# Performance work log

Hardware: AMD Instinct MI355X
Metric: run time of the kernel (lower is better)

## Reference

```python
import jax, jax.numpy as jnp
import numpy as np

# DeepSeek-V2 MLA dims (one tensor-parallel shard of 8)
H = 5120          # hidden size
S = 2048          # seq len
B = 1
NH = 16           # 128 heads / 8 devices
Q_LORA = 1536
KV_LORA = 512
NOPE = 128
ROPE = 64
QK = NOPE + ROPE  # 192 per-head q/k dim
VD = 128          # v head dim
DEVICE_NUM = 8
EPS = 1e-6


def rms_norm(x, w):
    v = jnp.mean(jnp.square(x.astype(jnp.float32)), axis=-1, keepdims=True)
    return (x * jax.lax.rsqrt(v + EPS)).astype(x.dtype) * w


def rope_cos_sin(position_ids, dim=ROPE, base=10000.0):
    inv_freq = 1.0 / (base ** (jnp.arange(0, dim, 2, dtype=jnp.float32) / dim))
    freqs = position_ids.astype(jnp.float32)[..., None] * inv_freq       # [B,S,dim/2]
    emb = jnp.concatenate([freqs, freqs], axis=-1)                        # [B,S,dim]
    return jnp.cos(emb), jnp.sin(emb)


def apply_rope(x, cos, sin):
    # DeepSeek interleaved reorder: view(b,h,s,d//2,2).transpose(-1,-2).reshape
    b, h, s, d = x.shape
    x = x.reshape(b, h, s, d // 2, 2).transpose(0, 1, 2, 4, 3).reshape(b, h, s, d)
    x1, x2 = x[..., : d // 2], x[..., d // 2:]
    rot = jnp.concatenate([-x2, x1], axis=-1)
    return x * cos[:, None] + rot * sin[:, None]


def setup_inputs() -> dict:
    key = jax.random.key(0)
    ks = jax.random.split(key, 8)
    sc = 0.02
    hidden_states = jax.random.normal(ks[0], (B, S, H), dtype=jnp.float32)
    position_ids = jnp.arange(S, dtype=jnp.int64 if jax.config.jax_enable_x64 else jnp.int32)[None, :].repeat(B, 0)
    attention_mask = jnp.triu(jnp.full((S, S), -1e9, dtype=jnp.float32), 1)[None, None]
    return {
        "hidden_states": hidden_states,
        "position_ids": position_ids,
        "attention_mask": attention_mask,
        "ln_w": jnp.ones((H,), jnp.float32),
        "q_a_w": jax.random.normal(ks[1], (Q_LORA, H), jnp.float32) * sc,
        "q_a_ln_w": jnp.ones((Q_LORA,), jnp.float32),
        "q_b_w": jax.random.normal(ks[2], (NH * QK, Q_LORA), jnp.float32) * sc,
        "kv_a_w": jax.random.normal(ks[3], (KV_LORA + ROPE, H), jnp.float32) * sc,
        "kv_a_ln_w": jnp.ones((KV_LORA,), jnp.float32),
        "kv_b_w": jax.random.normal(ks[4], (NH * (NOPE + VD), KV_LORA), jnp.float32) * sc,
        "o_w": jax.random.normal(ks[5], (H, NH * VD), jnp.float32) * sc,
    }


def reference(hidden_states, position_ids, attention_mask, ln_w, q_a_w, q_a_ln_w,
              q_b_w, kv_a_w, kv_a_ln_w, kv_b_w, o_w):
    b, s, _ = hidden_states.shape
    residual = hidden_states * (1.0 / DEVICE_NUM)
    x = rms_norm(hidden_states, ln_w)

    # Q path: low-rank down-proj + RMSNorm + up-proj
    q = rms_norm(x @ q_a_w.T, q_a_ln_w) @ q_b_w.T                # [b,s,NH*QK]
    q = q.reshape(b, s, NH, QK).transpose(0, 2, 1, 3)            # [b,NH,s,QK]
    q_nope, q_pe = q[..., :NOPE], q[..., NOPE:]

    # KV path: compressed latent + shared rope key
    ckv = x @ kv_a_w.T                                           # [b,s,KV_LORA+ROPE]
    c_kv, k_pe = ckv[..., :KV_LORA], ckv[..., KV_LORA:]
    k_pe = k_pe.reshape(b, s, 1, ROPE).transpose(0, 2, 1, 3)     # [b,1,s,ROPE]
    kv = rms_norm(c_kv, kv_a_ln_w) @ kv_b_w.T                    # [b,s,NH*(NOPE+VD)]
    kv = kv.reshape(b, s, NH, NOPE + VD).transpose(0, 2, 1, 3)
    k_nope, v = kv[..., :NOPE], kv[..., NOPE:]

    cos, sin = rope_cos_sin(position_ids)
    q_pe = apply_rope(q_pe, cos, sin)
    k_pe = apply_rope(k_pe, cos, sin)

    k = jnp.concatenate([k_nope, jnp.broadcast_to(k_pe, (b, NH, s, ROPE))], axis=-1)
    qf = jnp.concatenate([q_nope, q_pe], axis=-1)

    scores = jnp.einsum('bhqd,bhkd->bhqk', qf, k) * (1.0 / np.sqrt(QK))
    scores = scores + attention_mask
    probs = jax.nn.softmax(scores, axis=-1)
    attn = jnp.einsum('bhqk,bhkd->bhqd', probs, v)               # [b,NH,s,VD]

    out = attn.transpose(0, 2, 1, 3).reshape(b, s, NH * VD) @ o_w.T
    hidden = residual + out
    return hidden.astype(jnp.float32), k.astype(jnp.float32), v.astype(jnp.float32)
```

## Files before the change

### kernel.cpp

```cpp
#include <hip/hip_runtime.h>
#include <math.h>

typedef unsigned short u16;
typedef unsigned int u32;
typedef __attribute__((ext_vector_type(8))) short short8;
typedef __attribute__((ext_vector_type(4))) float f32x4;

#define NHEADS 16
static const int S      = 2048;
static const int Hd     = 5120;
static const int QLORA  = 1536;
static const int KVLORA = 512;
static const int NQK    = 192;
static const int NVD    = 128;
static const int QDIM   = 3072;
static const int KVDIM  = 4096;
static const int NFUSE  = 2176;

__device__ __forceinline__ u16 f2bf(float f) {
    union { float f; u32 u; } v; v.f = f;
    u32 r = v.u + 0x7FFFu + ((v.u >> 16) & 1u);
    return (u16)(r >> 16);
}

__global__ void convert_bf16_kernel(const float* __restrict__ src, u16* __restrict__ dst,
                                    int n_src, int n_total) {
    int i = (blockIdx.x * 256 + threadIdx.x) * 4;
    if (i >= n_total) return;
    union { u16 h[4]; uint2 u; } p;
    if (i < n_src) {
        float4 v = *(const float4*)(src + i);
        p.h[0] = f2bf(v.x); p.h[1] = f2bf(v.y); p.h[2] = f2bf(v.z); p.h[3] = f2bf(v.w);
    } else {
        p.h[0] = p.h[1] = p.h[2] = p.h[3] = 0;
    }
    *(uint2*)(dst + i) = p.u;
}

__global__ void rmsnorm_bf16_kernel(const float* in, const float* __restrict__ w,
                                    u16* out, int D, int in_stride, int out_stride) {
    int row = blockIdx.x;
    const float* x = in + (size_t)row * in_stride;
    u16* y = out + (size_t)row * out_stride;
    float ss = 0.f;
    for (int i = threadIdx.x; i < D; i += blockDim.x) { float v = x[i]; ss += v * v; }
    #pragma unroll
    for (int off = 32; off > 0; off >>= 1) ss += __shfl_xor(ss, off);
    __shared__ float wsum[8];
    int wid = threadIdx.x >> 6, lane = threadIdx.x & 63;
    if (lane == 0) wsum[wid] = ss;
    __syncthreads();
    float tot = 0.f;
    int nw = blockDim.x >> 6;
    for (int i = 0; i < nw; ++i) tot += wsum[i];
    float scale = rsqrtf(tot / (float)D + 1e-6f);
    for (int i = threadIdx.x; i < D; i += blockDim.x) y[i] = f2bf(x[i] * scale * w[i]);
}

__global__ __launch_bounds__(256) void gemm_bf16_kernel(
    const u16* __restrict__ A, const u16* __restrict__ B, float* __restrict__ C,
    int M, int N, int K, const float* __restrict__ resid) {
    __shared__ u16 As[4][128 * 32];
    __shared__ u16 Bs[4][128 * 32];

    const int lin = blockIdx.x + blockIdx.y * gridDim.x;
    const int nwg = gridDim.x * gridDim.y;
    const int xcd = lin & 7, off = lin >> 3;
    const int q = nwg >> 3, r = nwg & 7;
    const int wg = (xcd < r ? xcd * (q + 1) : r * (q + 1) + (xcd - r) * q) + off;
    const int bm = (wg % gridDim.y) * 128;
    const int bn = (wg / gridDim.y) * 128;

    const int tid = threadIdx.x;
    const int w = tid >> 6, lane = tid & 63;
    const int wr = w >> 1, wc = w & 1;
    const int fr = lane & 15, kg = lane >> 4;

    f32x4 acc[4][4];
    #pragma unroll
    for (int i = 0; i < 4; ++i)
        #pragma unroll
        for (int j = 0; j < 4; ++j) acc[i][j] = (f32x4){0.f, 0.f, 0.f, 0.f};

    const int srow = lane >> 2;
    const int scol = (lane & 3) * 8;
    const u16* Ap0 = A + (size_t)(bm + w * 32 + srow) * K + scol;
    const u16* Ap1 = Ap0 + (size_t)16 * K;
    const u16* Bp0 = B + (size_t)(bn + w * 32 + srow) * K + scol;
    const u16* Bp1 = Bp0 + (size_t)16 * K;
    const int ld0 = (w * 32) * 32;
    const int ld1 = (w * 32 + 16) * 32;

#define GSTAGE(buf, kk) do {                                                                  \
    __builtin_amdgcn_global_load_lds(                                                         \
        (const __attribute__((address_space(1))) void*)(Ap0 + (kk)),                          \
        (__attribute__((address_space(3))) void*)&As[buf][ld0], 16, 0, 0);                    \
    __builtin_amdgcn_global_load_lds(                                                         \
        (const __attribute__((address_space(1))) void*)(Ap1 + (kk)),                          \
        (__attribute__((address_space(3))) void*)&As[buf][ld1], 16, 0, 0);                    \
    __builtin_amdgcn_global_load_lds(                                                         \
        (const __attribute__((address_space(1))) void*)(Bp0 + (kk)),                          \
        (__attribute__((address_space(3))) void*)&Bs[buf][ld0], 16, 0, 0);                    \
    __builtin_amdgcn_global_load_lds(                                                         \
        (const __attribute__((address_space(1))) void*)(Bp1 + (kk)),                          \
        (__attribute__((address_space(3))) void*)&Bs[buf][ld1], 16, 0, 0);                    \
  } while (0)

#define GCOMP(buf) do {                                                                       \
    short8 af[4], bfr[4];                                                                     \
    _Pragma("unroll")                                                                         \
    for (int i = 0; i < 4; ++i) {                                                             \
      af[i]  = *(const short8*)&As[buf][(wr * 64 + i * 16 + fr) * 32 + kg * 8];               \
      bfr[i] = *(const short8*)&Bs[buf][(wc * 64 + i * 16 + fr) * 32 + kg * 8];               \
    }                                                                                         \
    _Pragma("unroll")                                                                         \
    for (int mi = 0; mi < 4; ++mi)                                                            \
      _Pragma("unroll")                                                                       \
      for (int ni = 0; ni < 4; ++ni)                                                          \
        acc[mi][ni] = __builtin_amdgcn_mfma_f32_16x16x32_bf16(af[mi], bfr[ni],                \
                                                              acc[mi][ni], 0, 0, 0);         \
  } while (0)

    const int nk = K >> 5;
    GSTAGE(0, 0);
    GSTAGE(1, 32);
    for (int kt = 0; kt < nk; ++kt) {
        if (kt + 2 < nk) {
            GSTAGE((kt + 2) & 3, (kt + 2) << 5);
            asm volatile("s_waitcnt vmcnt(8)" ::: "memory");
        } else if (kt + 1 < nk) {
            asm volatile("s_waitcnt vmcnt(4)" ::: "memory");
        } else {
            asm volatile("s_waitcnt vmcnt(0)" ::: "memory");
        }
        __builtin_amdgcn_s_barrier();
        GCOMP(kt & 3);
    }
#undef GSTAGE
#undef GCOMP

    #pragma unroll
    for (int mi = 0; mi < 4; ++mi)
        #pragma unroll
        for (int ni = 0; ni < 4; ++ni)
            #pragma unroll
            for (int r2 = 0; r2 < 4; ++r2) {
                int row = bm + wr * 64 + mi * 16 + kg * 4 + r2;
                int col = bn + wc * 64 + ni * 16 + fr;
                size_t idx = (size_t)row * N + col;
                float v = acc[mi][ni][r2];
                if (resid) v += resid[idx] * 0.125f;
                C[idx] = v;
            }
}

__global__ void prep_q_kernel(const float* __restrict__ Qb, const int* __restrict__ pos,
                              u16* __restrict__ Qbf) {
    const int s = blockIdx.x;
    const int t = threadIdx.x;
    const float* qrow = Qb + (size_t)s * QDIM;
    {
        int i = t * 4;
        int hh = i >> 7, d = i & 127;
        float4 v = *(const float4*)(qrow + hh * NQK + d);
        u16 p[4] = {f2bf(v.x), f2bf(v.y), f2bf(v.z), f2bf(v.w)};
        *(uint2*)(Qbf + ((size_t)hh * S + s) * NQK + d) = *(uint2*)p;
    }
    {
        int hh = t >> 5, j = t & 31;
        float ps = (float)pos[s];
        float inv_freq = 1.0f / powf(10000.0f, (float)j * (1.0f / 32.0f));
        float ang = ps * inv_freq;
        float c = cosf(ang), sn = sinf(ang);
        const float* pe = qrow + hh * NQK + 128;
        float a = pe[2 * j], b = pe[2 * j + 1];
        u16* dst = Qbf + ((size_t)hh * S + s) * NQK;
        dst[128 + j] = f2bf(a * c - b * sn);
        dst[160 + j] = f2bf(b * c + a * sn);
    }
}

__global__ void build_kv_kernel(const float* __restrict__ KV, const float* __restrict__ CKV,
                                int ckv_stride, const int* __restrict__ pos_ids,
                                float* __restrict__ Kout, float* __restrict__ Vout,
                                u16* __restrict__ Kbf) {
    int s = blockIdx.x;
    int t = threadIdx.x;
    __shared__ float kp[64];
    if (t < 32) {
        int j = t;
        float pos = (float)pos_ids[s];
        float inv_freq = 1.0f / powf(10000.0f, (float)j * (1.0f / 32.0f));
        float ang = pos * inv_freq;
        float c = cosf(ang), sn = sinf(ang);
        const float* kpe = CKV + (size_t)s * ckv_stride + KVLORA;
        float a = kpe[2 * j], b = kpe[2 * j + 1];
        kp[j] = a * c - b * sn;
        kp[32 + j] = b * c + a * sn;
    }
    __syncthreads();
    const float* kvrow = KV + (size_t)s * KVDIM;
    for (int i = t; i < NHEADS * NQK; i += 256) {
        int h = i / NQK, d = i % NQK;
        float v = (d < 128) ? kvrow[h * 256 + d] : kp[d - 128];
        size_t idx = ((size_t)h * S + s) * NQK + d;
        Kout[idx] = v;
        Kbf[idx] = f2bf(v);
    }
    for (int i = t; i < NHEADS * NVD; i += 256) {
        int h = i >> 7, d = i & 127;
        Vout[((size_t)h * S + s) * NVD + d] = kvrow[h * 256 + 128 + d];
    }
}

__global__ __launch_bounds__(256) void vt_kernel(const float* __restrict__ V, u16* __restrict__ Vt) {
    const int h = blockIdx.y;
    const int s0 = blockIdx.x * 64;
    const int t = threadIdx.x;
    __shared__ u16 T[64][132];
    #pragma unroll
    for (int j = 0; j < 8; ++j) {
        int f = t + j * 256;
        int row = f >> 5, c4 = f & 31;
        float4 v = *(const float4*)(V + ((size_t)h * S + s0 + row) * NVD + c4 * 4);
        u16 p[4] = {f2bf(v.x), f2bf(v.y), f2bf(v.z), f2bf(v.w)};
        *(uint2*)&T[row][c4 * 4] = *(uint2*)p;
    }
    __syncthreads();
    const int d = t >> 1, half = t & 1;
    #pragma unroll
    for (int c = 0; c < 4; ++c) {
        u16 tmp[8];
        #pragma unroll
        for (int e = 0; e < 8; ++e) tmp[e] = T[half * 32 + c * 8 + e][d];
        *(uint4*)(Vt + ((size_t)h * NVD + d) * S + s0 + half * 32 + c * 8) = *(uint4*)tmp;
    }
}

__global__ __launch_bounds__(256) void attn_mfma_kernel(
    const u16* __restrict__ Qbf, const u16* __restrict__ Kb,
    const u16* __restrict__ Vtb, u16* __restrict__ ATb) {
    const int h = blockIdx.y;
    const int q0 = blockIdx.x * 64;
    const int tid = threadIdx.x;
    const int w = tid >> 6, lane = tid & 63;
    const int fr = lane & 15, kg = lane >> 4;

    __shared__ __align__(16) u16 Ks[64 * 192];
    __shared__ __align__(16) u16 Vts[128 * 64];

    int kSrc[6], vSrc[4];
    #pragma unroll
    for (int i = 0; i < 6; ++i) {
        int D = (w * 6 + i) * 1024 + lane * 16;
        int row = D / 384, wb = D - row * 384;
        kSrc[i] = row * 384 + (wb ^ ((row & 7) << 4));
    }
    #pragma unroll
    for (int i = 0; i < 4; ++i) {
        int D = (w * 4 + i) * 1024 + lane * 16;
        int row = D >> 7, wb = D & 127;
        vSrc[i] = row * (S * 2) + (wb ^ ((row & 7) << 4));
    }
    const char* Kg = (const char*)(Kb + (size_t)h * S * NQK);
    const char* Vg = (const char*)(Vtb + (size_t)h * NVD * S);

    short8 qf[6];
    {
        const u16* qrow = Qbf + ((size_t)h * S + q0 + w * 16 + fr) * NQK;
        #pragma unroll
        for (int kb = 0; kb < 6; ++kb)
            qf[kb] = *(const short8*)(qrow + kb * 32 + kg * 8);
    }

    f32x4 o[8];
    #pragma unroll
    for (int ni = 0; ni < 8; ++ni) o[ni] = (f32x4){0.f, 0.f, 0.f, 0.f};
    float mrow = -1e30f, lrow = 0.f;
    const float scale = 0.0721687836487032f;
    const int qg = q0 + w * 16 + fr;
    const int swz = (fr & 7) << 4;

    for (int k0 = 0; k0 <= q0; k0 += 64) {
        __syncthreads();
        #pragma unroll
        for (int i = 0; i < 6; ++i)
            __builtin_amdgcn_global_load_lds(
                (const __attribute__((address_space(1))) void*)(Kg + (size_t)k0 * 384 + kSrc[i]),
                (__attribute__((address_space(3))) void*)((char*)Ks + (w * 6 + i) * 1024), 16, 0, 0);
        #pragma unroll
        for (int i = 0; i < 4; ++i)
            __builtin_amdgcn_global_load_lds(
                (const __attribute__((address_space(1))) void*)(Vg + (size_t)k0 * 2 + vSrc[i]),
                (__attribute__((address_space(3))) void*)((char*)Vts + (w * 4 + i) * 1024), 16, 0, 0);
        __syncthreads();

        f32x4 sacc[4];
        #pragma unroll
        for (int mi = 0; mi < 4; ++mi) sacc[mi] = (f32x4){0.f, 0.f, 0.f, 0.f};
        #pragma unroll
        for (int mi = 0; mi < 4; ++mi)
            #pragma unroll
            for (int kb = 0; kb < 6; ++kb) {
                const short8 kf = *(const short8*)((const char*)Ks +
                    (mi * 16 + fr) * 384 + ((kb * 64 + kg * 16) ^ swz));
                sacc[mi] = __builtin_amdgcn_mfma_f32_16x16x32_bf16(kf, qf[kb], sacc[mi], 0, 0, 0);
            }

        const bool diag = (k0 == q0);
        float p[4][4];
        float mx = -1e30f;
        #pragma unroll
        for (int mi = 0; mi < 4; ++mi)
            #pragma unroll
            for (int r = 0; r < 4; ++r) {
                float v = sacc[mi][r] * scale;
                if (diag && (k0 + mi * 16 + kg * 4 + r > qg)) v = -1e30f;
                p[mi][r] = v;
                mx = fmaxf(mx, v);
            }
        mx = fmaxf(mx, __shfl_xor(mx, 16));
        mx = fmaxf(mx, __shfl_xor(mx, 32));
        float mnew = fmaxf(mrow, mx);
        float corr = __expf(mrow - mnew);
        float psum = 0.f;
        #pragma unroll
        for (int mi = 0; mi < 4; ++mi)
            #pragma unroll
            for (int r = 0; r < 4; ++r) {
                float e = __expf(p[mi][r] - mnew);
                p[mi][r] = e;
                psum += e;
            }
        psum += __shfl_xor(psum, 16);
        psum += __shfl_xor(psum, 32);
        lrow = lrow * corr + psum;
        mrow = mnew;
        float corr_r[4];
        #pragma unroll
        for (int r = 0; r < 4; ++r) corr_r[r] = __shfl(corr, kg * 4 + r);
        #pragma unroll
        for (int ni = 0; ni < 8; ++ni) {
            o[ni][0] *= corr_r[0]; o[ni][1] *= corr_r[1];
            o[ni][2] *= corr_r[2]; o[ni][3] *= corr_r[3];
        }

        u32 pk0[4], pk1[4];
        #pragma unroll
        for (int mi = 0; mi < 4; ++mi) {
            pk0[mi] = (u32)f2bf(p[mi][0]) | ((u32)f2bf(p[mi][1]) << 16);
            pk1[mi] = (u32)f2bf(p[mi][2]) | ((u32)f2bf(p[mi][3]) << 16);
        }
        const int srcA = 2 * (kg & 1) * 16 + fr;
        const int srcB = srcA + 16;
        const int hsel = kg >> 1;
        short8 pa[2];
        #pragma unroll
        for (int ks = 0; ks < 2; ++ks) {
            u32 a0 = (u32)__shfl((int)pk0[ks * 2], srcA), b0 = (u32)__shfl((int)pk0[ks * 2 + 1], srcA);
            u32 a1 = (u32)__shfl((int)pk1[ks * 2], srcA), b1 = (u32)__shfl((int)pk1[ks * 2 + 1], srcA);
            u32 a2 = (u32)__shfl((int)pk0[ks * 2], srcB), b2 = (u32)__shfl((int)pk0[ks * 2 + 1], srcB);
            u32 a3 = (u32)__shfl((int)pk1[ks * 2], srcB), b3 = (u32)__shfl((int)pk1[ks * 2 + 1], srcB);
            union { u32 u[4]; short8 s8; } cvt;
            cvt.u[0] = hsel ? b0 : a0;
            cvt.u[1] = hsel ? b1 : a1;
            cvt.u[2] = hsel ? b2 : a2;
            cvt.u[3] = hsel ? b3 : a3;
            pa[ks] = cvt.s8;
        }

        #pragma unroll
        for (int ks = 0; ks < 2; ++ks)
            #pragma unroll
            for (int ni = 0; ni < 8; ++ni) {
                const short8 vf = *(const short8*)((const char*)Vts +
                    (ni * 16 + fr) * 128 + ((ks * 64 + kg * 16) ^ swz));
                o[ni] = __builtin_amdgcn_mfma_f32_16x16x32_bf16(pa[ks], vf, o[ni], 0, 0, 0);
            }
    }

    float inv = 1.f / lrow;
    float inv_r[4];
    #pragma unroll
    for (int r = 0; r < 4; ++r) inv_r[r] = __shfl(inv, kg * 4 + r);
    u16* outp = ATb + (size_t)(q0 + w * 16 + kg * 4) * (NHEADS * NVD) + h * NVD + fr;
    #pragma unroll
    for (int ni = 0; ni < 8; ++ni)
        #pragma unroll
        for (int r = 0; r < 4; ++r)
            outp[(size_t)r * (NHEADS * NVD) + ni * 16] = f2bf(o[ni][r] * inv_r[r]);
}

extern "C" void kernel_launch(void* const* d_in, const int* in_sizes, int n_in,
                              void* d_out, int out_size, void* d_ws, size_t ws_size,
                              hipStream_t stream) {
    (void)in_sizes; (void)n_in; (void)out_size; (void)ws_size;
    const float* hidden    = (const float*)d_in[0];
    const int*   pos       = (const int*)d_in[1];
    const float* ln_w      = (const float*)d_in[3];
    const float* q_a_w     = (const float*)d_in[4];
    const float* q_a_ln_w  = (const float*)d_in[5];
    const float* q_b_w     = (const float*)d_in[6];
    const float* kv_a_w    = (const float*)d_in[7];
    const float* kv_a_ln_w = (const float*)d_in[8];
    const float* kv_b_w    = (const float*)d_in[9];
    const float* o_w       = (const float*)d_in[10];

    float* OUT_H = (float*)d_out;
    float* OUT_K = OUT_H + (size_t)S * Hd;
    float* OUT_V = OUT_K + (size_t)NHEADS * S * NQK;

    char* ws = (char*)d_ws;
    u16*   o_wb    = (u16*)(ws);
    u16*   Wf      = (u16*)(ws + 20971520);
    u16*   Xb      = (u16*)(ws + 43253760);
    float* CF      = (float*)(ws + 64225280);
    u16*   QAn     = (u16*)(ws + 82055680);
    u16*   q_b_wb  = (u16*)(ws + 88347136);
    float* Qb      = (float*)(ws + 20971520);
    u16*   kv_b_wb = (u16*)(ws + 46137344);
    u16*   CKVN    = (u16*)(ws + 82055680);
    float* KV      = (float*)(ws + 84152832);
    u16*   Qbf     = (u16*)(ws + 50331648);
    u16*   Kbf     = (u16*)(ws + 20971520);
    u16*   Vtb     = (u16*)(ws + 33554432);
    u16*   ATb     = (u16*)(ws + 64225280);

    convert_bf16_kernel<<<(Hd * 2048 / 4 + 255) / 256, 256, 0, stream>>>(o_w, o_wb, Hd * 2048, Hd * 2048);
    convert_bf16_kernel<<<(QLORA * Hd / 4 + 255) / 256, 256, 0, stream>>>(q_a_w, Wf, QLORA * Hd, QLORA * Hd);
    convert_bf16_kernel<<<(640 * Hd / 4 + 255) / 256, 256, 0, stream>>>(kv_a_w, Wf + (size_t)QLORA * Hd, 576 * Hd, 640 * Hd);

    rmsnorm_bf16_kernel<<<S, 256, 0, stream>>>(hidden, ln_w, Xb, Hd, Hd, Hd);
    gemm_bf16_kernel<<<dim3(NFUSE / 128, S / 128), 256, 0, stream>>>(Xb, Wf, CF, S, NFUSE, Hd, nullptr);
    convert_bf16_kernel<<<(KVDIM * KVLORA / 4 + 255) / 256, 256, 0, stream>>>(kv_b_w, kv_b_wb, KVDIM * KVLORA, KVDIM * KVLORA);
    rmsnorm_bf16_kernel<<<S, 256, 0, stream>>>(CF, q_a_ln_w, QAn, QLORA, NFUSE, QLORA);
    convert_bf16_kernel<<<(QDIM * QLORA / 4 + 255) / 256, 256, 0, stream>>>(q_b_w, q_b_wb, QDIM * QLORA, QDIM * QLORA);
    gemm_bf16_kernel<<<dim3(QDIM / 128, S / 128), 256, 0, stream>>>(QAn, q_b_wb, Qb, S, QDIM, QLORA, nullptr);
    rmsnorm_bf16_kernel<<<S, 256, 0, stream>>>(CF + QLORA, kv_a_ln_w, CKVN, KVLORA, NFUSE, KVLORA);
    gemm_bf16_kernel<<<dim3(KVDIM / 128, S / 128), 256, 0, stream>>>(CKVN, kv_b_wb, KV, S, KVDIM, KVLORA, nullptr);
    prep_q_kernel<<<S, 512, 0, stream>>>(Qb, pos, Qbf);
    build_kv_kernel<<<S, 256, 0, stream>>>(KV, CF + QLORA, NFUSE, pos, OUT_K, OUT_V, Kbf);
    vt_kernel<<<dim3(S / 64, NHEADS), 256, 0, stream>>>(OUT_V, Vtb);
    attn_mfma_kernel<<<dim3(S / 64, NHEADS), 256, 0, stream>>>(Qbf, Kbf, Vtb, ATb);
    gemm_bf16_kernel<<<dim3(Hd / 128, S / 128), 256, 0, stream>>>(ATb, o_wb, OUT_H, S, Hd, NHEADS * NVD, hidden);
}
```

Before: 445.2 us.

## Emit bf16 intermediates from GEMMs, fuse K/V build with V transpose, add BM=64 tiles

```diff
diff --git a/kernel.cpp b/kernel.cpp
--- a/kernel.cpp
+++ b/kernel.cpp
@@ -22,6 +22,9 @@
     u32 r = v.u + 0x7FFFu + ((v.u >> 16) & 1u);
     return (u16)(r >> 16);
 }
+__device__ __forceinline__ float bf2f(u16 h) {
+    union { u32 u; float f; } v; v.u = (u32)h << 16; return v.f;
+}
 
 __global__ void convert_bf16_kernel(const float* __restrict__ src, u16* __restrict__ dst,
                                     int n_src, int n_total) {
@@ -57,114 +60,148 @@
     for (int i = threadIdx.x; i < D; i += blockDim.x) y[i] = f2bf(x[i] * scale * w[i]);
 }
 
-__global__ __launch_bounds__(256) void gemm_bf16_kernel(
-    const u16* __restrict__ A, const u16* __restrict__ B, float* __restrict__ C,
+__global__ void rmsnorm_bf16in_kernel(const u16* in, const float* __restrict__ w,
+                                      u16* out, int D, int in_stride, int out_stride) {
+    int row = blockIdx.x;
+    const u16* x = in + (size_t)row * in_stride;
+    u16* y = out + (size_t)row * out_stride;
+    float ss = 0.f;
+    for (int i = threadIdx.x; i < D; i += blockDim.x) { float v = bf2f(x[i]); ss += v * v; }
+    #pragma unroll
+    for (int off = 32; off > 0; off >>= 1) ss += __shfl_xor(ss, off);
+    __shared__ float wsum[8];
+    int wid = threadIdx.x >> 6, lane = threadIdx.x & 63;
+    if (lane == 0) wsum[wid] = ss;
+    __syncthreads();
+    float tot = 0.f;
+    int nw = blockDim.x >> 6;
+    for (int i = 0; i < nw; ++i) tot += wsum[i];
+    float scale = rsqrtf(tot / (float)D + 1e-6f);
+    for (int i = threadIdx.x; i < D; i += blockDim.x) y[i] = f2bf(bf2f(x[i]) * scale * w[i]);
+}
+
+template<int BM, bool SWZ, bool OBF>
+__global__ __launch_bounds__(256) void gemm_k(
+    const u16* __restrict__ A, const u16* __restrict__ B, void* __restrict__ Cv,
     int M, int N, int K, const float* __restrict__ resid) {
-    __shared__ u16 As[4][128 * 32];
+    constexpr int MR = BM / 32;
+    __shared__ u16 As[4][BM * 32];
     __shared__ u16 Bs[4][128 * 32];
 
-    const int lin = blockIdx.x + blockIdx.y * gridDim.x;
-    const int nwg = gridDim.x * gridDim.y;
-    const int xcd = lin & 7, off = lin >> 3;
-    const int q = nwg >> 3, r = nwg & 7;
-    const int wg = (xcd < r ? xcd * (q + 1) : r * (q + 1) + (xcd - r) * q) + off;
-    const int bm = (wg % gridDim.y) * 128;
-    const int bn = (wg / gridDim.y) * 128;
+    int bm, bn;
+    if constexpr (SWZ) {
+        const int lin = blockIdx.x + blockIdx.y * gridDim.x;
+        const int nwg = gridDim.x * gridDim.y;
+        const int xcd = lin & 7, off = lin >> 3;
+        const int q = nwg >> 3, r = nwg & 7;
+        const int wg = (xcd < r ? xcd * (q + 1) : r * (q + 1) + (xcd - r) * q) + off;
+        bm = (wg % gridDim.y) * BM;
+        bn = (wg / gridDim.y) * 128;
+    } else {
+        bm = blockIdx.y * BM;
+        bn = blockIdx.x * 128;
+    }
 
     const int tid = threadIdx.x;
     const int w = tid >> 6, lane = tid & 63;
     const int wr = w >> 1, wc = w & 1;
     const int fr = lane & 15, kg = lane >> 4;
 
-    f32x4 acc[4][4];
-    #pragma unroll
-    for (int i = 0; i < 4; ++i)
+    f32x4 acc[MR][4];
+    #pragma unroll
+    for (int i = 0; i < MR; ++i)
         #pragma unroll
         for (int j = 0; j < 4; ++j) acc[i][j] = (f32x4){0.f, 0.f, 0.f, 0.f};
 
     const int srow = lane >> 2;
     const int scol = (lane & 3) * 8;
-    const u16* Ap0 = A + (size_t)(bm + w * 32 + srow) * K + scol;
+    const u16* Ap0 = A + (size_t)(bm + w * (BM / 4) + srow) * K + scol;
     const u16* Ap1 = Ap0 + (size_t)16 * K;
     const u16* Bp0 = B + (size_t)(bn + w * 32 + srow) * K + scol;
     const u16* Bp1 = Bp0 + (size_t)16 * K;
-    const int ld0 = (w * 32) * 32;
-    const int ld1 = (w * 32 + 16) * 32;
-
-#define GSTAGE(buf, kk) do {                                                                  \
-    __builtin_amdgcn_global_load_lds(                                                         \
-        (const __attribute__((address_space(1))) void*)(Ap0 + (kk)),                          \
-        (__attribute__((address_space(3))) void*)&As[buf][ld0], 16, 0, 0);                    \
-    __builtin_amdgcn_global_load_lds(                                                         \
-        (const __attribute__((address_space(1))) void*)(Ap1 + (kk)),                          \
-        (__attribute__((address_space(3))) void*)&As[buf][ld1], 16, 0, 0);                    \
-    __builtin_amdgcn_global_load_lds(                                                         \
-        (const __attribute__((address_space(1))) void*)(Bp0 + (kk)),                          \
-        (__attribute__((address_space(3))) void*)&Bs[buf][ld0], 16, 0, 0);                    \
-    __builtin_amdgcn_global_load_lds(                                                         \
-        (const __attribute__((address_space(1))) void*)(Bp1 + (kk)),                          \
-        (__attribute__((address_space(3))) void*)&Bs[buf][ld1], 16, 0, 0);                    \
-  } while (0)
-
-#define GCOMP(buf) do {                                                                       \
-    short8 af[4], bfr[4];                                                                     \
-    _Pragma("unroll")                                                                         \
-    for (int i = 0; i < 4; ++i) {                                                             \
-      af[i]  = *(const short8*)&As[buf][(wr * 64 + i * 16 + fr) * 32 + kg * 8];               \
-      bfr[i] = *(const short8*)&Bs[buf][(wc * 64 + i * 16 + fr) * 32 + kg * 8];               \
-    }                                                                                         \
-    _Pragma("unroll")                                                                         \
-    for (int mi = 0; mi < 4; ++mi)                                                            \
-      _Pragma("unroll")                                                                       \
-      for (int ni = 0; ni < 4; ++ni)                                                          \
-        acc[mi][ni] = __builtin_amdgcn_mfma_f32_16x16x32_bf16(af[mi], bfr[ni],                \
-                                                              acc[mi][ni], 0, 0, 0);         \
-  } while (0)
+    const int lda0 = (w * (BM / 4)) * 32;
+    const int lda1 = (w * (BM / 4) + 16) * 32;
+    const int ldb0 = (w * 32) * 32;
+    const int ldb1 = (w * 32 + 16) * 32;
+
+    auto STAGE = [&](int buf, int kk) {
+        __builtin_amdgcn_global_load_lds(
+            (const __attribute__((address_space(1))) void*)(Ap0 + kk),
+            (__attribute__((address_space(3))) void*)&As[buf][lda0], 16, 0, 0);
+        if constexpr (BM == 128)
+            __builtin_amdgcn_global_load_lds(
+                (const __attribute__((address_space(1))) void*)(Ap1 + kk),
+                (__attribute__((address_space(3))) void*)&As[buf][lda1], 16, 0, 0);
+        __builtin_amdgcn_global_load_lds(
+            (const __attribute__((address_space(1))) void*)(Bp0 + kk),
+            (__attribute__((address_space(3))) void*)&Bs[buf][ldb0], 16, 0, 0);
+        __builtin_amdgcn_global_load_lds(
+            (const __attribute__((address_space(1))) void*)(Bp1 + kk),
+            (__attribute__((address_space(3))) void*)&Bs[buf][ldb1], 16, 0, 0);
+    };
+    auto COMP = [&](int buf) {
+        short8 af[MR], bfr[4];
+        #pragma unroll
+        for (int i = 0; i < MR; ++i)
+            af[i] = *(const short8*)&As[buf][(wr * (BM / 2) + i * 16 + fr) * 32 + kg * 8];
+        #pragma unroll
+        for (int i = 0; i < 4; ++i)
+            bfr[i] = *(const short8*)&Bs[buf][(wc * 64 + i * 16 + fr) * 32 + kg * 8];
+        #pragma unroll
+        for (int mi = 0; mi < MR; ++mi)
+            #pragma unroll
+            for (int ni = 0; ni < 4; ++ni)
+                acc[mi][ni] = __builtin_amdgcn_mfma_f32_16x16x32_bf16(af[mi], bfr[ni],
+                                                                      acc[mi][ni], 0, 0, 0);
+    };
 
     const int nk = K >> 5;
-    GSTAGE(0, 0);
-    GSTAGE(1, 32);
+    STAGE(0, 0);
+    STAGE(1, 32);
     for (int kt = 0; kt < nk; ++kt) {
         if (kt + 2 < nk) {
-            GSTAGE((kt + 2) & 3, (kt + 2) << 5);
-            asm volatile("s_waitcnt vmcnt(8)" ::: "memory");
+            STAGE((kt + 2) & 3, (kt + 2) << 5);
+            if constexpr (BM == 128) asm volatile("s_waitcnt vmcnt(8)" ::: "memory");
+            else                     asm volatile("s_waitcnt vmcnt(6)" ::: "memory");
         } else if (kt + 1 < nk) {
-            asm volatile("s_waitcnt vmcnt(4)" ::: "memory");
+            if constexpr (BM == 128) asm volatile("s_waitcnt vmcnt(4)" ::: "memory");
+            else                     asm volatile("s_waitcnt vmcnt(3)" ::: "memory");
         } else {
             asm volatile("s_waitcnt vmcnt(0)" ::: "memory");
         }
         __builtin_amdgcn_s_barrier();
-        GCOMP(kt & 3);
-    }
-#undef GSTAGE
-#undef GCOMP
-
-    #pragma unroll
-    for (int mi = 0; mi < 4; ++mi)
+        COMP(kt & 3);
+    }
+
+    #pragma unroll
+    for (int mi = 0; mi < MR; ++mi)
         #pragma unroll
         for (int ni = 0; ni < 4; ++ni)
             #pragma unroll
             for (int r2 = 0; r2 < 4; ++r2) {
-                int row = bm + wr * 64 + mi * 16 + kg * 4 + r2;
+                int row = bm + wr * (BM / 2) + mi * 16 + kg * 4 + r2;
                 int col = bn + wc * 64 + ni * 16 + fr;
                 size_t idx = (size_t)row * N + col;
                 float v = acc[mi][ni][r2];
-                if (resid) v += resid[idx] * 0.125f;
-                C[idx] = v;
+                if constexpr (OBF) {
+                    ((u16*)Cv)[idx] = f2bf(v);
+                } else {
+                    if (resid) v += resid[idx] * 0.125f;
+                    ((float*)Cv)[idx] = v;
+                }
             }
 }
 
-__global__ void prep_q_kernel(const float* __restrict__ Qb, const int* __restrict__ pos,
+__global__ void prep_q_kernel(const u16* __restrict__ Qb, const int* __restrict__ pos,
                               u16* __restrict__ Qbf) {
     const int s = blockIdx.x;
     const int t = threadIdx.x;
-    const float* qrow = Qb + (size_t)s * QDIM;
+    const u16* qrow = Qb + (size_t)s * QDIM;
     {
         int i = t * 4;
         int hh = i >> 7, d = i & 127;
-        float4 v = *(const float4*)(qrow + hh * NQK + d);
-        u16 p[4] = {f2bf(v.x), f2bf(v.y), f2bf(v.z), f2bf(v.w)};
-        *(uint2*)(Qbf + ((size_t)hh * S + s) * NQK + d) = *(uint2*)p;
+        uint2 v = *(const uint2*)(qrow + hh * NQK + d);
+        *(uint2*)(Qbf + ((size_t)hh * S + s) * NQK + d) = v;
     }
     {
         int hh = t >> 5, j = t & 31;
@@ -172,59 +209,71 @@
         float inv_freq = 1.0f / powf(10000.0f, (float)j * (1.0f / 32.0f));
         float ang = ps * inv_freq;
         float c = cosf(ang), sn = sinf(ang);
-        const float* pe = qrow + hh * NQK + 128;
-        float a = pe[2 * j], b = pe[2 * j + 1];
+        const u16* pe = qrow + hh * NQK + 128;
+        float a = bf2f(pe[2 * j]), b = bf2f(pe[2 * j + 1]);
         u16* dst = Qbf + ((size_t)hh * S + s) * NQK;
         dst[128 + j] = f2bf(a * c - b * sn);
         dst[160 + j] = f2bf(b * c + a * sn);
     }
 }
 
-__global__ void build_kv_kernel(const float* __restrict__ KV, const float* __restrict__ CKV,
-                                int ckv_stride, const int* __restrict__ pos_ids,
-                                float* __restrict__ Kout, float* __restrict__ Vout,
-                                u16* __restrict__ Kbf) {
-    int s = blockIdx.x;
-    int t = threadIdx.x;
-    __shared__ float kp[64];
-    if (t < 32) {
-        int j = t;
-        float pos = (float)pos_ids[s];
+__global__ __launch_bounds__(256) void build_kv64_kernel(
+    const u16* __restrict__ KVb, const u16* __restrict__ CF,
+    const int* __restrict__ pos_ids,
+    float* __restrict__ Kout, float* __restrict__ Vout,
+    u16* __restrict__ Kbf, u16* __restrict__ Vtb) {
+    const int s0 = blockIdx.x * 64;
+    const int h  = blockIdx.y;
+    const int t  = threadIdx.x;
+    __shared__ u16 T[64][132];
+
+    #pragma unroll
+    for (int it = 0; it < 4; ++it) {
+        int i = t + it * 256;
+        int row = i >> 4, c8 = (i & 15) * 8;
+        int s = s0 + row;
+        union { uint4 u; u16 hx[8]; } v;
+        v.u = *(const uint4*)(KVb + (size_t)s * KVDIM + h * 256 + c8);
+        size_t kidx = ((size_t)h * S + s) * NQK + c8;
+        *(uint4*)(Kbf + kidx) = v.u;
+        float4 f0 = {bf2f(v.hx[0]), bf2f(v.hx[1]), bf2f(v.hx[2]), bf2f(v.hx[3])};
+        float4 f1 = {bf2f(v.hx[4]), bf2f(v.hx[5]), bf2f(v.hx[6]), bf2f(v.hx[7])};
+        *(float4*)(Kout + kidx) = f0;
+        *(float4*)(Kout + kidx + 4) = f1;
+    }
+    #pragma unroll
+    for (int it = 0; it < 4; ++it) {
+        int i = t + it * 256;
+        int row = i >> 4, c8 = (i & 15) * 8;
+        int s = s0 + row;
+        union { uint4 u; uint2 d[2]; u16 hx[8]; } v;
+        v.u = *(const uint4*)(KVb + (size_t)s * KVDIM + h * 256 + 128 + c8);
+        *(uint2*)&T[row][c8]     = v.d[0];
+        *(uint2*)&T[row][c8 + 4] = v.d[1];
+        size_t vidx = ((size_t)h * S + s) * NVD + c8;
+        float4 f0 = {bf2f(v.hx[0]), bf2f(v.hx[1]), bf2f(v.hx[2]), bf2f(v.hx[3])};
+        float4 f1 = {bf2f(v.hx[4]), bf2f(v.hx[5]), bf2f(v.hx[6]), bf2f(v.hx[7])};
+        *(float4*)(Vout + vidx) = f0;
+        *(float4*)(Vout + vidx + 4) = f1;
+    }
+    #pragma unroll
+    for (int it = 0; it < 8; ++it) {
+        int i = t + it * 256;
+        int row = i >> 5, j = i & 31;
+        int s = s0 + row;
+        float ps = (float)pos_ids[s];
         float inv_freq = 1.0f / powf(10000.0f, (float)j * (1.0f / 32.0f));
-        float ang = pos * inv_freq;
+        float ang = ps * inv_freq;
         float c = cosf(ang), sn = sinf(ang);
-        const float* kpe = CKV + (size_t)s * ckv_stride + KVLORA;
-        float a = kpe[2 * j], b = kpe[2 * j + 1];
-        kp[j] = a * c - b * sn;
-        kp[32 + j] = b * c + a * sn;
-    }
-    __syncthreads();
-    const float* kvrow = KV + (size_t)s * KVDIM;
-    for (int i = t; i < NHEADS * NQK; i += 256) {
-        int h = i / NQK, d = i % NQK;
-        float v = (d < 128) ? kvrow[h * 256 + d] : kp[d - 128];
-        size_t idx = ((size_t)h * S + s) * NQK + d;
-        Kout[idx] = v;
-        Kbf[idx] = f2bf(v);
-    }
-    for (int i = t; i < NHEADS * NVD; i += 256) {
-        int h = i >> 7, d = i & 127;
-        Vout[((size_t)h * S + s) * NVD + d] = kvrow[h * 256 + 128 + d];
-    }
-}
-
-__global__ __launch_bounds__(256) void vt_kernel(const float* __restrict__ V, u16* __restrict__ Vt) {
-    const int h = blockIdx.y;
-    const int s0 = blockIdx.x * 64;
-    const int t = threadIdx.x;
-    __shared__ u16 T[64][132];
-    #pragma unroll
-    for (int j = 0; j < 8; ++j) {
-        int f = t + j * 256;
-        int row = f >> 5, c4 = f & 31;
-        float4 v = *(const float4*)(V + ((size_t)h * S + s0 + row) * NVD + c4 * 4);
-        u16 p[4] = {f2bf(v.x), f2bf(v.y), f2bf(v.z), f2bf(v.w)};
-        *(uint2*)&T[row][c4 * 4] = *(uint2*)p;
+        u32 pr = *(const u32*)(CF + (size_t)s * NFUSE + QLORA + KVLORA + 2 * j);
+        float a = bf2f((u16)pr), b = bf2f((u16)(pr >> 16));
+        float k0 = a * c - b * sn;
+        float k1 = b * c + a * sn;
+        size_t kidx = ((size_t)h * S + s) * NQK;
+        Kout[kidx + 128 + j] = k0;
+        Kout[kidx + 160 + j] = k1;
+        Kbf[kidx + 128 + j] = f2bf(k0);
+        Kbf[kidx + 160 + j] = f2bf(k1);
     }
     __syncthreads();
     const int d = t >> 1, half = t & 1;
@@ -233,7 +282,7 @@
         u16 tmp[8];
         #pragma unroll
         for (int e = 0; e < 8; ++e) tmp[e] = T[half * 32 + c * 8 + e][d];
-        *(uint4*)(Vt + ((size_t)h * NVD + d) * S + s0 + half * 32 + c * 8) = *(uint4*)tmp;
+        *(uint4*)(Vtb + ((size_t)h * NVD + d) * S + s0 + half * 32 + c * 8) = *(uint4*)tmp;
     }
 }
 
@@ -413,34 +462,33 @@
     char* ws = (char*)d_ws;
     u16*   o_wb    = (u16*)(ws);
     u16*   Wf      = (u16*)(ws + 20971520);
+    u16*   Qbf     = (u16*)(ws + 20971520);
+    u16*   Vtb     = (u16*)(ws + 33554432);
     u16*   Xb      = (u16*)(ws + 43253760);
-    float* CF      = (float*)(ws + 64225280);
-    u16*   QAn     = (u16*)(ws + 82055680);
-    u16*   q_b_wb  = (u16*)(ws + 88347136);
-    float* Qb      = (float*)(ws + 20971520);
-    u16*   kv_b_wb = (u16*)(ws + 46137344);
-    u16*   CKVN    = (u16*)(ws + 82055680);
-    float* KV      = (float*)(ws + 84152832);
-    u16*   Qbf     = (u16*)(ws + 50331648);
-    u16*   Kbf     = (u16*)(ws + 20971520);
-    u16*   Vtb     = (u16*)(ws + 33554432);
-    u16*   ATb     = (u16*)(ws + 64225280);
+    u16*   Kbf     = (u16*)(ws + 43253760);
+    u16*   ATb     = (u16*)(ws + 55836672);
+    u16*   CF      = (u16*)(ws + 64225280);
+    u16*   QAn     = (u16*)(ws + 73138176);
+    u16*   CKVN    = (u16*)(ws + 73138176);
+    u16*   q_b_wb  = (u16*)(ws + 79429632);
+    u16*   kv_b_wb = (u16*)(ws + 79429632);
+    u16*   KVb     = (u16*)(ws + 88866816);
+    u16*   Qb      = (u16*)(ws + 105644032);
 
     convert_bf16_kernel<<<(Hd * 2048 / 4 + 255) / 256, 256, 0, stream>>>(o_w, o_wb, Hd * 2048, Hd * 2048);
     convert_bf16_kernel<<<(QLORA * Hd / 4 + 255) / 256, 256, 0, stream>>>(q_a_w, Wf, QLORA * Hd, QLORA * Hd);
     convert_bf16_kernel<<<(640 * Hd / 4 + 255) / 256, 256, 0, stream>>>(kv_a_w, Wf + (size_t)QLORA * Hd, 576 * Hd, 640 * Hd);
 
     rmsnorm_bf16_kernel<<<S, 256, 0, stream>>>(hidden, ln_w, Xb, Hd, Hd, Hd);
-    gemm_bf16_kernel<<<dim3(NFUSE / 128, S / 128), 256, 0, stream>>>(Xb, Wf, CF, S, NFUSE, Hd, nullptr);
+    gemm_k<128, true, true><<<dim3(NFUSE / 128, S / 128), 256, 0, stream>>>(Xb, Wf, CF, S, NFUSE, Hd, nullptr);
+    convert_bf16_kernel<<<(QDIM * QLORA / 4 + 255) / 256, 256, 0, stream>>>(q_b_w, q_b_wb, QDIM * QLORA, QDIM * QLORA);
+    rmsnorm_bf16in_kernel<<<S, 256, 0, stream>>>(CF, q_a_ln_w, QAn, QLORA, NFUSE, QLORA);
+    gemm_k<128, true, true><<<dim3(QDIM / 128, S / 128), 256, 0, stream>>>(QAn, q_b_wb, Qb, S, QDIM, QLORA, nullptr);
     convert_bf16_kernel<<<(KVDIM * KVLORA / 4 + 255) / 256, 256, 0, stream>>>(kv_b_w, kv_b_wb, KVDIM * KVLORA, KVDIM * KVLORA);
-    rmsnorm_bf16_kernel<<<S, 256, 0, stream>>>(CF, q_a_ln_w, QAn, QLORA, NFUSE, QLORA);
-    convert_bf16_kernel<<<(QDIM * QLORA / 4 + 255) / 256, 256, 0, stream>>>(q_b_w, q_b_wb, QDIM * QLORA, QDIM * QLORA);
-    gemm_bf16_kernel<<<dim3(QDIM / 128, S / 128), 256, 0, stream>>>(QAn, q_b_wb, Qb, S, QDIM, QLORA, nullptr);
-    rmsnorm_bf16_kernel<<<S, 256, 0, stream>>>(CF + QLORA, kv_a_ln_w, CKVN, KVLORA, NFUSE, KVLORA);
-    gemm_bf16_kernel<<<dim3(KVDIM / 128, S / 128), 256, 0, stream>>>(CKVN, kv_b_wb, KV, S, KVDIM, KVLORA, nullptr);
+    rmsnorm_bf16in_kernel<<<S, 256, 0, stream>>>(CF + QLORA, kv_a_ln_w, CKVN, KVLORA, NFUSE, KVLORA);
+    gemm_k<64, false, true><<<dim3(KVDIM / 128, S / 64), 256, 0, stream>>>(CKVN, kv_b_wb, KVb, S, KVDIM, KVLORA, nullptr);
     prep_q_kernel<<<S, 512, 0, stream>>>(Qb, pos, Qbf);
-    build_kv_kernel<<<S, 256, 0, stream>>>(KV, CF + QLORA, NFUSE, pos, OUT_K, OUT_V, Kbf);
-    vt_kernel<<<dim3(S / 64, NHEADS), 256, 0, stream>>>(OUT_V, Vtb);
+    build_kv64_kernel<<<dim3(S / 64, NHEADS), 256, 0, stream>>>(KVb, CF, pos, OUT_K, OUT_V, Kbf, Vtb);
     attn_mfma_kernel<<<dim3(S / 64, NHEADS), 256, 0, stream>>>(Qbf, Kbf, Vtb, ATb);
-    gemm_bf16_kernel<<<dim3(Hd / 128, S / 128), 256, 0, stream>>>(ATb, o_wb, OUT_H, S, Hd, NHEADS * NVD, hidden);
-}
+    gemm_k<64, false, false><<<dim3(Hd / 128, S / 64), 256, 0, stream>>>(ATb, o_wb, OUT_H, S, Hd, NHEADS * NVD, hidden);
+}
```

Result: faster. 420.2 us (-5.6%).
